# Kernel optimization log

Measured on AMD Instinct MI355X. Metric: run time of the kernel, lower is better.

## Reference

```python
import jax, jax.numpy as jnp
import numpy as np

NUM_HEADS = 8
DIM_HEAD = 48
SCALE = DIM_HEAD ** -0.5


def setup_inputs() -> dict:
    key = jax.random.key(0)
    k1, k2, k3 = jax.random.split(key, 3)
    B, N, D = 4, 2048, 384
    inner = NUM_HEADS * DIM_HEAD  # 384
    x = jax.random.normal(k1, (B, N, D), dtype=jnp.float32)
    # store weights in [in, out] layout (equivalent to torch Linear W.T)
    Wqkv = jax.random.normal(k2, (D, 3 * inner), dtype=jnp.float32) * (D ** -0.5)
    Wproj = jax.random.normal(k3, (inner, D), dtype=jnp.float32) * (inner ** -0.5)
    bproj = jnp.zeros((D,), dtype=jnp.float32)
    return {"x": x, "Wqkv": Wqkv, "Wproj": Wproj, "bproj": bproj}


def reference(x, Wqkv, Wproj, bproj):
    B, N, D = x.shape
    h, dh = NUM_HEADS, DIM_HEAD
    C = h * dh
    # fused QKV projection (qkv_bias=False)
    qkv = (x @ Wqkv).reshape(B, N, 3, h, dh)
    q = qkv[:, :, 0].transpose(0, 2, 1, 3)  # [B, h, N, dh]
    k = qkv[:, :, 1].transpose(0, 2, 1, 3)
    v = qkv[:, :, 2].transpose(0, 2, 1, 3)
    # naive attention: materialize [B, h, N, N] scores
    sim = jnp.einsum("bhqd,bhkd->bhqk", q, k) * SCALE
    attn = jax.nn.softmax(sim, axis=-1)
    out = jnp.einsum("bhqk,bhkd->bhqd", attn, v)  # [B, h, N, dh]
    out = out.transpose(0, 2, 1, 3).reshape(B, N, C)
    return out @ Wproj + bproj
```

## Files before the change

### kernel.cpp

```cpp
#include <hip/hip_runtime.h>
#include <hip/hip_bf16.h>


typedef _Float16 f16x8 __attribute__((ext_vector_type(8)));
typedef _Float16 f16x4 __attribute__((ext_vector_type(4)));
typedef _Float16 f16x2 __attribute__((ext_vector_type(2)));
typedef float    f32x4 __attribute__((ext_vector_type(4)));
typedef float    f32x16 __attribute__((ext_vector_type(16)));

#define QSCL 0.20822035963448658f

static __device__ __forceinline__ f16x2 cvt_pk_f16(float a, float b) {
    return __builtin_bit_cast(f16x2, __builtin_amdgcn_cvt_pkrtz(a, b));
}

__global__ __launch_bounds__(256) void prep(const float4* __restrict__ x,
                                            const float* __restrict__ wq,
                                            const float* __restrict__ wp,
                                            f16x4* __restrict__ xh4,
                                            _Float16* __restrict__ wqt,
                                            _Float16* __restrict__ wpt)
{
    __shared__ _Float16 t[64][65];
    const int blk = blockIdx.x, tid = threadIdx.x;
    if (blk < 144) {
        const float* src; _Float16* dst; int Nn, k0, n0;
        if (blk < 108) {
            src = wq; dst = wqt; Nn = 1152;
            k0 = (blk % 6) * 64; n0 = (blk / 6) * 64;
        } else {
            const int b2 = blk - 108;
            src = wp; dst = wpt; Nn = 384;
            k0 = (b2 % 6) * 64; n0 = (b2 / 6) * 64;
        }
        #pragma unroll
        for (int i = 0; i < 16; i++) {
            const int id = tid + i * 256;
            const int k = id >> 6, n = id & 63;
            t[k][n] = (_Float16)src[(size_t)(k0 + k) * Nn + n0 + n];
        }
        __syncthreads();
        #pragma unroll
        for (int i = 0; i < 16; i++) {
            const int id = tid + i * 256;
            const int n = id >> 6, k = id & 63;
            dst[(size_t)(n0 + n) * 384 + k0 + k] = t[k][n];
        }
    } else {
        const int base = (blk - 144) * 3072;
        #pragma unroll
        for (int r = 0; r < 12; r++) {
            const int j = base + r * 256 + tid;
            const float4 tt = x[j];
            f16x4 hh;
            hh[0] = (_Float16)tt.x; hh[1] = (_Float16)tt.y;
            hh[2] = (_Float16)tt.z; hh[3] = (_Float16)tt.w;
            xh4[j] = hh;
        }
    }
}

union QkvSmem {
    struct { _Float16 As[128][40]; _Float16 Bs[128][40]; } g;
    _Float16 Ts[128][136];
    _Float16 Ts2[128][136];
};

__global__ __launch_bounds__(256) void qkv_f16(const _Float16* __restrict__ A,
                                               const _Float16* __restrict__ Bt,
                                               _Float16* __restrict__ qh,
                                               _Float16* __restrict__ kh,
                                               _Float16* __restrict__ vt)
{
    __shared__ QkvSmem sm;
    const int tid = threadIdx.x;
    const int w = tid >> 6, lane = tid & 63, cl = lane & 15, quad = lane >> 4;
    const int bm = blockIdx.x, bn = blockIdx.y;

    f32x4 acc[2][8];
    const f32x4 z4 = {0.f, 0.f, 0.f, 0.f};
    #pragma unroll
    for (int mi = 0; mi < 2; mi++)
        #pragma unroll
        for (int t = 0; t < 8; t++) acc[mi][t] = z4;

    const int ar = tid >> 2, ac = (tid & 3) * 8;
    const _Float16* Ag = A  + (size_t)(bm * 128 + ar) * 384 + ac;
    const _Float16* Bg = Bt + (size_t)(bn * 128 + ar) * 384 + ac;

    f16x8 pa[2], pb[2];
    #pragma unroll
    for (int j = 0; j < 2; j++) {
        pa[j] = *(const f16x8*)(Ag + (size_t)(64 * j) * 384);
        pb[j] = *(const f16x8*)(Bg + (size_t)(64 * j) * 384);
    }

    for (int k0 = 0; k0 < 384; k0 += 32) {
        __syncthreads();
        #pragma unroll
        for (int j = 0; j < 2; j++) {
            *(f16x8*)&sm.g.As[ar + 64 * j][ac] = pa[j];
            *(f16x8*)&sm.g.Bs[ar + 64 * j][ac] = pb[j];
        }
        __syncthreads();
        if (k0 + 32 < 384) {
            #pragma unroll
            for (int j = 0; j < 2; j++) {
                pa[j] = *(const f16x8*)(Ag + (size_t)(64 * j) * 384 + k0 + 32);
                pb[j] = *(const f16x8*)(Bg + (size_t)(64 * j) * 384 + k0 + 32);
            }
        }
        f16x8 bf[8];
        #pragma unroll
        for (int t = 0; t < 8; t++)
            bf[t] = *(const f16x8*)&sm.g.Bs[t * 16 + cl][quad * 8];
        #pragma unroll
        for (int mi = 0; mi < 2; mi++) {
            const f16x8 af = *(const f16x8*)&sm.g.As[w * 32 + mi * 16 + cl][quad * 8];
            #pragma unroll
            for (int t = 0; t < 8; t++)
                acc[mi][t] = __builtin_amdgcn_mfma_f32_16x16x32_f16(af, bf[t], acc[mi][t], 0, 0, 0);
        }
    }

    const int s = (bn * 128) / 384;
    const int b  = (bm * 128) >> 11;
    const int n0 = (bm * 128) & 2047;
    if (s == 2) {
        __syncthreads();
        const int qp = ((quad & 1) << 1) | (quad >> 1);
        #pragma unroll
        for (int t = 0; t < 8; t++)
            #pragma unroll
            for (int mi = 0; mi < 2; mi++)
                #pragma unroll
                for (int r = 0; r < 4; r++)
                    sm.Ts[t * 16 + cl][w * 32 + mi * 16 + qp * 4 + r] =
                        (_Float16)acc[mi][t][r];
        __syncthreads();
        const int colbase = bn * 128 - 768;
        #pragma unroll
        for (int i = 0; i < 8; i++) {
            const int c = i * 256 + tid;
            const int col = c >> 4, nc = c & 15;
            const int gcol = colbase + col;
            const int head = gcol / 48, d = gcol - head * 48;
            const int bh = b * 8 + head;
            *(f16x8*)&vt[(size_t)(bh * 48 + d) * 2048 + n0 + nc * 8] =
                *(const f16x8*)&sm.Ts[col][nc * 8];
        }
    } else {
        __syncthreads();
        const float scl = (s == 0) ? QSCL : 1.0f;
        #pragma unroll
        for (int t = 0; t < 8; t++)
            #pragma unroll
            for (int mi = 0; mi < 2; mi++)
                #pragma unroll
                for (int r = 0; r < 4; r++)
                    sm.Ts2[w * 32 + mi * 16 + quad * 4 + r][t * 16 + cl] =
                        (_Float16)(acc[mi][t][r] * scl);
        __syncthreads();
        _Float16* dst = (s == 0) ? qh : kh;
        const int colbase = bn * 128 - s * 384;
        #pragma unroll
        for (int i = 0; i < 8; i++) {
            const int c = i * 256 + tid;
            const int row = c >> 4, ch = c & 15;
            const int gcol = colbase + ch * 8;
            const int head = gcol / 48, d = gcol - head * 48;
            const int bh = b * 8 + head;
            *(f16x8*)&dst[(size_t)(bh * 2048 + n0 + row) * 48 + d] =
                *(const f16x8*)&sm.Ts2[row][ch * 8];
        }
    }
}

#define KS_S 56
#define VS_S 72

union AttnSmem {
    struct {
        _Float16 Ks[2][2][64][KS_S];
        _Float16 Vts[2][2][64][VS_S];
    } a;
    struct {
        float    Of[128][52];
        float    lv[128];
        _Float16 Ot[128][58];
    } e;
};

__global__ __launch_bounds__(512) void attn_f16(const _Float16* __restrict__ qh,
                                                const _Float16* __restrict__ kh,
                                                const _Float16* __restrict__ vt,
                                                _Float16* __restrict__ ab)
{
    __shared__ AttnSmem sm;
    const int tid = threadIdx.x;
    const int w = tid >> 6, lane = tid & 63, ln = lane & 31, h = lane >> 5;
    const int g = w >> 2, wg = w & 3;
    const int tid2 = tid & 255;
    const int bh = blockIdx.x, qt = blockIdx.y;

    for (int i = tid; i < 2 * 2 * 16 * VS_S; i += 512) {
        const int gi = i / (2 * 16 * VS_S);
        const int j  = i - gi * (2 * 16 * VS_S);
        const int bi = j / (16 * VS_S);
        const int j2 = j - bi * (16 * VS_S);
        const int r = 48 + j2 / VS_S, c = j2 % VS_S;
        sm.a.Vts[gi][bi][r][c] = (r == 48) ? (_Float16)1.0f : (_Float16)0.0f;
    }

    f16x8 qf[3];
    {
        const _Float16* qp = qh + (size_t)(bh * 2048 + qt * 128 + wg * 32 + ln) * 48 + 8 * h;
        qf[0] = *(const f16x8*)qp;
        qf[1] = *(const f16x8*)(qp + 16);
        qf[2] = *(const f16x8*)(qp + 32);
    }

    f32x16 o0, o1;
    #pragma unroll
    for (int r = 0; r < 16; r++) { o0[r] = 0.f; o1[r] = 0.f; }

    const _Float16* kbase = kh + (size_t)bh * 2048 * 48 + (size_t)g * 1024 * 48;
    const _Float16* vbase = vt + (size_t)bh * 48 * 2048 + g * 1024;

    const int kr0 = tid2 / 6,        kc0 = (tid2 % 6) * 8;
    const int kid1 = tid2 + 256;
    const int kr1 = kid1 / 6,        kc1 = (kid1 % 6) * 8;
    const int vr0 = tid2 >> 3,       vc0 = (tid2 & 7) * 8;
    const int vr1 = vr0 + 32;
    const _Float16* ks0 = kbase + (size_t)kr0 * 48 + kc0;
    const _Float16* ks1 = kbase + (size_t)kr1 * 48 + kc1;
    const _Float16* vs0 = vbase + (size_t)vr0 * 2048 + vc0;
    const _Float16* vs1 = vbase + (size_t)vr1 * 2048 + vc0;

    f16x8 rk0 = *(const f16x8*)ks0;
    f16x8 rv0 = *(const f16x8*)vs0;
    f16x8 rk1, rv1;
    if (tid2 < 128) { rk1 = *(const f16x8*)ks1; rv1 = *(const f16x8*)vs1; }

    for (int t = 0; t < 16; ++t) {
        _Float16 (*Ksb)[KS_S] = sm.a.Ks[g][t & 1];
        _Float16 (*Vtb)[VS_S] = sm.a.Vts[g][t & 1];

        *(f16x8*)&Ksb[kr0][kc0] = rk0;
        *(f16x8*)&Vtb[vr0][vc0] = rv0;
        if (tid2 < 128) {
            *(f16x8*)&Ksb[kr1][kc1] = rk1;
            *(f16x8*)&Vtb[vr1][vc0] = rv1;
        }
        __syncthreads();

        if (t < 15) {
            const int off = (t + 1) * 64;
            rk0 = *(const f16x8*)(ks0 + (size_t)off * 48);
            rv0 = *(const f16x8*)(vs0 + off);
            if (tid2 < 128) {
                rk1 = *(const f16x8*)(ks1 + (size_t)off * 48);
                rv1 = *(const f16x8*)(vs1 + off);
            }
        }

        f32x16 s0, s1;
        #pragma unroll
        for (int r = 0; r < 16; r++) { s0[r] = 0.f; s1[r] = 0.f; }
        __builtin_amdgcn_s_setprio(1);
        #pragma unroll
        for (int i = 0; i < 3; i++) {
            const f16x8 ka0 = *(const f16x8*)&Ksb[ln][16 * i + 8 * h];
            s0 = __builtin_amdgcn_mfma_f32_32x32x16_f16(ka0, qf[i], s0, 0, 0, 0);
            const f16x8 ka1 = *(const f16x8*)&Ksb[32 + ln][16 * i + 8 * h];
            s1 = __builtin_amdgcn_mfma_f32_32x32x16_f16(ka1, qf[i], s1, 0, 0, 0);
        }
        __builtin_amdgcn_s_setprio(0);

        f16x8 pbf[4];
        f16x2* pp = (f16x2*)pbf;
        #pragma unroll
        for (int m = 0; m < 4; m++) {
            pp[m]      = cvt_pk_f16(
                __builtin_amdgcn_exp2f(s0[2 * m]),     __builtin_amdgcn_exp2f(s0[2 * m + 1]));
            pp[4 + m]  = cvt_pk_f16(
                __builtin_amdgcn_exp2f(s0[8 + 2 * m]), __builtin_amdgcn_exp2f(s0[9 + 2 * m]));
            pp[8 + m]  = cvt_pk_f16(
                __builtin_amdgcn_exp2f(s1[2 * m]),     __builtin_amdgcn_exp2f(s1[2 * m + 1]));
            pp[12 + m] = cvt_pk_f16(
                __builtin_amdgcn_exp2f(s1[8 + 2 * m]), __builtin_amdgcn_exp2f(s1[9 + 2 * m]));
        }

        __builtin_amdgcn_s_setprio(1);
        #pragma unroll
        for (int c = 0; c < 4; c++) {
            const f16x8 av0 = *(const f16x8*)&Vtb[ln][16 * c + 8 * h];
            o0 = __builtin_amdgcn_mfma_f32_32x32x16_f16(av0, pbf[c], o0, 0, 0, 0);
            const f16x8 av1 = *(const f16x8*)&Vtb[32 + ln][16 * c + 8 * h];
            o1 = __builtin_amdgcn_mfma_f32_32x32x16_f16(av1, pbf[c], o1, 0, 0, 0);
        }
        __builtin_amdgcn_s_setprio(0);
    }

    const float lown = __shfl(o1[8], ln);

    __syncthreads();

    const int row = wg * 32 + ln;
    if (g == 1) {
        #pragma unroll
        for (int q4 = 0; q4 < 4; q4++) {
            f32x4 tq = { o0[4 * q4], o0[4 * q4 + 1], o0[4 * q4 + 2], o0[4 * q4 + 3] };
            *(f32x4*)&sm.e.Of[row][8 * q4 + 4 * h] = tq;
        }
        #pragma unroll
        for (int q4 = 0; q4 < 2; q4++) {
            f32x4 tq = { o1[4 * q4], o1[4 * q4 + 1], o1[4 * q4 + 2], o1[4 * q4 + 3] };
            *(f32x4*)&sm.e.Of[row][32 + 8 * q4 + 4 * h] = tq;
        }
        if (h == 0) sm.e.lv[row] = o1[8];
    }
    __syncthreads();
    if (g == 0) {
        #pragma unroll
        for (int q4 = 0; q4 < 4; q4++) {
            const f32x4 tq = *(const f32x4*)&sm.e.Of[row][8 * q4 + 4 * h];
            o0[4 * q4] += tq[0]; o0[4 * q4 + 1] += tq[1];
            o0[4 * q4 + 2] += tq[2]; o0[4 * q4 + 3] += tq[3];
        }
        #pragma unroll
        for (int q4 = 0; q4 < 2; q4++) {
            const f32x4 tq = *(const f32x4*)&sm.e.Of[row][32 + 8 * q4 + 4 * h];
            o1[4 * q4] += tq[0]; o1[4 * q4 + 1] += tq[1];
            o1[4 * q4 + 2] += tq[2]; o1[4 * q4 + 3] += tq[3];
        }
        const float inv = 1.f / (lown + sm.e.lv[row]);
        #pragma unroll
        for (int r = 0; r < 16; r++)
            sm.e.Ot[row][(r & 3) + 8 * (r >> 2) + 4 * h] = (_Float16)(o0[r] * inv);
        #pragma unroll
        for (int r = 0; r < 8; r++)
            sm.e.Ot[row][32 + (r & 3) + 8 * (r >> 2) + 4 * h] = (_Float16)(o1[r] * inv);
    }
    __syncthreads();
    if (g == 0) {
        const int b = bh >> 3, hd = bh & 7;
        #pragma unroll
        for (int i = 0; i < 3; i++) {
            const int c2 = i * 256 + tid;
            const int rw = c2 / 6, ch = c2 % 6;
            const int q = qt * 128 + rw;
            *(f16x8*)&ab[(size_t)(b * 2048 + q) * 384 + hd * 48 + ch * 8] =
                *(const f16x8*)&sm.e.Ot[rw][ch * 8];
        }
    }
}

__global__ __launch_bounds__(256) void proj_f16(const _Float16* __restrict__ A,
                                                const _Float16* __restrict__ Bt,
                                                const float* __restrict__ bias,
                                                float* __restrict__ out)
{
    __shared__ _Float16 As[64][72];
    __shared__ _Float16 Bs[64][72];
    const int tid = threadIdx.x;
    const int w = tid >> 6, lane = tid & 63, cl = lane & 15, quad = lane >> 4;
    const int bm = blockIdx.x, bn = blockIdx.y;

    f32x4 acc[4];
    const f32x4 z4 = {0.f, 0.f, 0.f, 0.f};
    #pragma unroll
    for (int t = 0; t < 4; t++) acc[t] = z4;

    const int ar = tid >> 3, ac = (tid & 7) * 8;
    const _Float16* Ag = A  + (size_t)(bm * 64 + ar) * 384 + ac;
    const _Float16* Bg = Bt + (size_t)(bn * 64 + ar) * 384 + ac;

    f16x8 pa[2], pb[2];
    #pragma unroll
    for (int j = 0; j < 2; j++) {
        pa[j] = *(const f16x8*)(Ag + (size_t)(32 * j) * 384);
        pb[j] = *(const f16x8*)(Bg + (size_t)(32 * j) * 384);
    }

    for (int k0 = 0; k0 < 384; k0 += 64) {
        __syncthreads();
        #pragma unroll
        for (int j = 0; j < 2; j++) {
            *(f16x8*)&As[ar + 32 * j][ac] = pa[j];
            *(f16x8*)&Bs[ar + 32 * j][ac] = pb[j];
        }
        __syncthreads();
        if (k0 + 64 < 384) {
            #pragma unroll
            for (int j = 0; j < 2; j++) {
                pa[j] = *(const f16x8*)(Ag + (size_t)(32 * j) * 384 + k0 + 64);
                pb[j] = *(const f16x8*)(Bg + (size_t)(32 * j) * 384 + k0 + 64);
            }
        }
        #pragma unroll
        for (int kh2 = 0; kh2 < 2; kh2++) {
            const f16x8 af = *(const f16x8*)&As[w * 16 + cl][kh2 * 32 + quad * 8];
            #pragma unroll
            for (int t = 0; t < 4; t++) {
                const f16x8 bf = *(const f16x8*)&Bs[t * 16 + cl][kh2 * 32 + quad * 8];
                acc[t] = __builtin_amdgcn_mfma_f32_16x16x32_f16(af, bf, acc[t], 0, 0, 0);
            }
        }
    }

    #pragma unroll
    for (int t = 0; t < 4; t++) {
        const int col = bn * 64 + t * 16 + cl;
        const float bv = bias[col];
        #pragma unroll
        for (int r = 0; r < 4; r++) {
            const int row = bm * 64 + w * 16 + quad * 4 + r;
            out[(size_t)row * 384 + col] = acc[t][r] + bv;
        }
    }
}

extern "C" void kernel_launch(void* const* d_in, const int* in_sizes, int n_in,
                              void* d_out, int out_size, void* d_ws, size_t ws_size,
                              hipStream_t stream) {
    const float* x     = (const float*)d_in[0];
    const float* Wqkv  = (const float*)d_in[1];
    const float* Wproj = (const float*)d_in[2];
    const float* bproj = (const float*)d_in[3];
    float* out = (float*)d_out;

    char* ws = (char*)d_ws;
    _Float16* xh     = (_Float16*)(ws + 0);
    _Float16* wqkvt  = (_Float16*)(ws + 6291456);
    _Float16* wprojt = (_Float16*)(ws + 7176192);
    _Float16* qh     = (_Float16*)(ws + 7471104);
    _Float16* kh     = (_Float16*)(ws + 13762560);
    _Float16* vt     = (_Float16*)(ws + 20054016);
    _Float16* ab     = (_Float16*)(ws + 26345472);

    prep<<<400, 256, 0, stream>>>((const float4*)x, Wqkv, Wproj,
                                  (f16x4*)xh, wqkvt, wprojt);
    qkv_f16<<<dim3(64, 9), 256, 0, stream>>>(xh, wqkvt, qh, kh, vt);
    attn_f16<<<dim3(32, 16), 512, 0, stream>>>(qh, kh, vt, ab);
    proj_f16<<<dim3(128, 6), 256, 0, stream>>>(ab, wprojt, bproj, out);
}
```

Baseline: 130.2 us.

## Double-buffer LDS tiles to halve barriers in QKV, attention and projection

The QKV GEMM and projection GEMM now use two LDS buffers for their tiles, as the attention kernel already did for K/V. Each iteration writes the next tile into the other buffer before computing on the current one, so only one __syncthreads per iteration is needed instead of two. The global prefetch distance is pushed one more tile ahead. The projection kernel's K-step drops from 64 to 32 to fit the new layout, which raises the iteration count and the number of barriers it executes, and the doubled LDS footprint may affect occupancy.

New measurement: 128.7 us (median of 3 runs). About the same (-1.1%).

```diff
diff --git a/kernel.cpp b/kernel.cpp
--- a/kernel.cpp
+++ b/kernel.cpp
@@ -61,7 +61,7 @@
 }
 
 union QkvSmem {
-    struct { _Float16 As[128][40]; _Float16 Bs[128][40]; } g;
+    struct { _Float16 As[2][128][40]; _Float16 Bs[2][128][40]; } g;
     _Float16 Ts[128][136];
     _Float16 Ts2[128][136];
 };
@@ -94,40 +94,52 @@
         pa[j] = *(const f16x8*)(Ag + (size_t)(64 * j) * 384);
         pb[j] = *(const f16x8*)(Bg + (size_t)(64 * j) * 384);
     }
-
-    for (int k0 = 0; k0 < 384; k0 += 32) {
-        __syncthreads();
-        #pragma unroll
-        for (int j = 0; j < 2; j++) {
-            *(f16x8*)&sm.g.As[ar + 64 * j][ac] = pa[j];
-            *(f16x8*)&sm.g.Bs[ar + 64 * j][ac] = pb[j];
-        }
-        __syncthreads();
-        if (k0 + 32 < 384) {
+    #pragma unroll
+    for (int j = 0; j < 2; j++) {
+        *(f16x8*)&sm.g.As[0][ar + 64 * j][ac] = pa[j];
+        *(f16x8*)&sm.g.Bs[0][ar + 64 * j][ac] = pb[j];
+    }
+    #pragma unroll
+    for (int j = 0; j < 2; j++) {
+        pa[j] = *(const f16x8*)(Ag + (size_t)(64 * j) * 384 + 32);
+        pb[j] = *(const f16x8*)(Bg + (size_t)(64 * j) * 384 + 32);
+    }
+    __syncthreads();
+
+    for (int it = 0; it < 12; ++it) {
+        if (it < 11) {
             #pragma unroll
             for (int j = 0; j < 2; j++) {
-                pa[j] = *(const f16x8*)(Ag + (size_t)(64 * j) * 384 + k0 + 32);
-                pb[j] = *(const f16x8*)(Bg + (size_t)(64 * j) * 384 + k0 + 32);
+                *(f16x8*)&sm.g.As[(it + 1) & 1][ar + 64 * j][ac] = pa[j];
+                *(f16x8*)&sm.g.Bs[(it + 1) & 1][ar + 64 * j][ac] = pb[j];
             }
+            if (it < 10) {
+                const int off = (it + 2) * 32;
+                #pragma unroll
+                for (int j = 0; j < 2; j++) {
+                    pa[j] = *(const f16x8*)(Ag + (size_t)(64 * j) * 384 + off);
+                    pb[j] = *(const f16x8*)(Bg + (size_t)(64 * j) * 384 + off);
+                }
+            }
         }
         f16x8 bf[8];
         #pragma unroll
         for (int t = 0; t < 8; t++)
-            bf[t] = *(const f16x8*)&sm.g.Bs[t * 16 + cl][quad * 8];
+            bf[t] = *(const f16x8*)&sm.g.Bs[it & 1][t * 16 + cl][quad * 8];
         #pragma unroll
         for (int mi = 0; mi < 2; mi++) {
-            const f16x8 af = *(const f16x8*)&sm.g.As[w * 32 + mi * 16 + cl][quad * 8];
+            const f16x8 af = *(const f16x8*)&sm.g.As[it & 1][w * 32 + mi * 16 + cl][quad * 8];
             #pragma unroll
             for (int t = 0; t < 8; t++)
                 acc[mi][t] = __builtin_amdgcn_mfma_f32_16x16x32_f16(af, bf[t], acc[mi][t], 0, 0, 0);
         }
+        __syncthreads();
     }
 
     const int s = (bn * 128) / 384;
     const int b  = (bm * 128) >> 11;
     const int n0 = (bm * 128) & 2047;
     if (s == 2) {
-        __syncthreads();
         const int qp = ((quad & 1) << 1) | (quad >> 1);
         #pragma unroll
         for (int t = 0; t < 8; t++)
@@ -150,7 +162,6 @@
                 *(const f16x8*)&sm.Ts[col][nc * 8];
         }
     } else {
-        __syncthreads();
         const float scl = (s == 0) ? QSCL : 1.0f;
         #pragma unroll
         for (int t = 0; t < 8; t++)
@@ -242,27 +253,47 @@
     f16x8 rk1, rv1;
     if (tid2 < 128) { rk1 = *(const f16x8*)ks1; rv1 = *(const f16x8*)vs1; }
 
-    for (int t = 0; t < 16; ++t) {
-        _Float16 (*Ksb)[KS_S] = sm.a.Ks[g][t & 1];
-        _Float16 (*Vtb)[VS_S] = sm.a.Vts[g][t & 1];
-
+    {
+        _Float16 (*Ksb)[KS_S] = sm.a.Ks[g][0];
+        _Float16 (*Vtb)[VS_S] = sm.a.Vts[g][0];
         *(f16x8*)&Ksb[kr0][kc0] = rk0;
         *(f16x8*)&Vtb[vr0][vc0] = rv0;
         if (tid2 < 128) {
             *(f16x8*)&Ksb[kr1][kc1] = rk1;
             *(f16x8*)&Vtb[vr1][vc0] = rv1;
         }
-        __syncthreads();
-
+        rk0 = *(const f16x8*)(ks0 + (size_t)64 * 48);
+        rv0 = *(const f16x8*)(vs0 + 64);
+        if (tid2 < 128) {
+            rk1 = *(const f16x8*)(ks1 + (size_t)64 * 48);
+            rv1 = *(const f16x8*)(vs1 + 64);
+        }
+        __syncthreads();
+    }
+
+    for (int t = 0; t < 16; ++t) {
         if (t < 15) {
-            const int off = (t + 1) * 64;
-            rk0 = *(const f16x8*)(ks0 + (size_t)off * 48);
-            rv0 = *(const f16x8*)(vs0 + off);
+            _Float16 (*Ksn)[KS_S] = sm.a.Ks[g][(t + 1) & 1];
+            _Float16 (*Vtn)[VS_S] = sm.a.Vts[g][(t + 1) & 1];
+            *(f16x8*)&Ksn[kr0][kc0] = rk0;
+            *(f16x8*)&Vtn[vr0][vc0] = rv0;
             if (tid2 < 128) {
-                rk1 = *(const f16x8*)(ks1 + (size_t)off * 48);
-                rv1 = *(const f16x8*)(vs1 + off);
+                *(f16x8*)&Ksn[kr1][kc1] = rk1;
+                *(f16x8*)&Vtn[vr1][vc0] = rv1;
             }
-        }
+            if (t < 14) {
+                const int off = (t + 2) * 64;
+                rk0 = *(const f16x8*)(ks0 + (size_t)off * 48);
+                rv0 = *(const f16x8*)(vs0 + off);
+                if (tid2 < 128) {
+                    rk1 = *(const f16x8*)(ks1 + (size_t)off * 48);
+                    rv1 = *(const f16x8*)(vs1 + off);
+                }
+            }
+        }
+
+        _Float16 (*Ksb)[KS_S] = sm.a.Ks[g][t & 1];
+        _Float16 (*Vtb)[VS_S] = sm.a.Vts[g][t & 1];
 
         f32x16 s0, s1;
         #pragma unroll
@@ -300,11 +331,11 @@
             o1 = __builtin_amdgcn_mfma_f32_32x32x16_f16(av1, pbf[c], o1, 0, 0, 0);
         }
         __builtin_amdgcn_s_setprio(0);
+
+        __syncthreads();
     }
 
     const float lown = __shfl(o1[8], ln);
-
-    __syncthreads();
 
     const int row = wg * 32 + ln;
     if (g == 1) {
@@ -361,8 +392,8 @@
                                                 const float* __restrict__ bias,
                                                 float* __restrict__ out)
 {
-    __shared__ _Float16 As[64][72];
-    __shared__ _Float16 Bs[64][72];
+    __shared__ _Float16 As[2][64][40];
+    __shared__ _Float16 Bs[2][64][40];
     const int tid = threadIdx.x;
     const int w = tid >> 6, lane = tid & 63, cl = lane & 15, quad = lane >> 4;
     const int bm = blockIdx.x, bn = blockIdx.y;
@@ -372,41 +403,35 @@
     #pragma unroll
     for (int t = 0; t < 4; t++) acc[t] = z4;
 
-    const int ar = tid >> 3, ac = (tid & 7) * 8;
+    const int ar = tid >> 2, ac = (tid & 3) * 8;
     const _Float16* Ag = A  + (size_t)(bm * 64 + ar) * 384 + ac;
     const _Float16* Bg = Bt + (size_t)(bn * 64 + ar) * 384 + ac;
 
-    f16x8 pa[2], pb[2];
-    #pragma unroll
-    for (int j = 0; j < 2; j++) {
-        pa[j] = *(const f16x8*)(Ag + (size_t)(32 * j) * 384);
-        pb[j] = *(const f16x8*)(Bg + (size_t)(32 * j) * 384);
-    }
-
-    for (int k0 = 0; k0 < 384; k0 += 64) {
-        __syncthreads();
-        #pragma unroll
-        for (int j = 0; j < 2; j++) {
-            *(f16x8*)&As[ar + 32 * j][ac] = pa[j];
-            *(f16x8*)&Bs[ar + 32 * j][ac] = pb[j];
-        }
-        __syncthreads();
-        if (k0 + 64 < 384) {
-            #pragma unroll
-            for (int j = 0; j < 2; j++) {
-                pa[j] = *(const f16x8*)(Ag + (size_t)(32 * j) * 384 + k0 + 64);
-                pb[j] = *(const f16x8*)(Bg + (size_t)(32 * j) * 384 + k0 + 64);
+    f16x8 pa = *(const f16x8*)Ag;
+    f16x8 pb = *(const f16x8*)Bg;
+    *(f16x8*)&As[0][ar][ac] = pa;
+    *(f16x8*)&Bs[0][ar][ac] = pb;
+    pa = *(const f16x8*)(Ag + 32);
+    pb = *(const f16x8*)(Bg + 32);
+    __syncthreads();
+
+    for (int it = 0; it < 12; ++it) {
+        if (it < 11) {
+            *(f16x8*)&As[(it + 1) & 1][ar][ac] = pa;
+            *(f16x8*)&Bs[(it + 1) & 1][ar][ac] = pb;
+            if (it < 10) {
+                const int off = (it + 2) * 32;
+                pa = *(const f16x8*)(Ag + off);
+                pb = *(const f16x8*)(Bg + off);
             }
         }
-        #pragma unroll
-        for (int kh2 = 0; kh2 < 2; kh2++) {
-            const f16x8 af = *(const f16x8*)&As[w * 16 + cl][kh2 * 32 + quad * 8];
-            #pragma unroll
-            for (int t = 0; t < 4; t++) {
-                const f16x8 bf = *(const f16x8*)&Bs[t * 16 + cl][kh2 * 32 + quad * 8];
-                acc[t] = __builtin_amdgcn_mfma_f32_16x16x32_f16(af, bf, acc[t], 0, 0, 0);
-            }
-        }
+        const f16x8 af = *(const f16x8*)&As[it & 1][w * 16 + cl][quad * 8];
+        #pragma unroll
+        for (int t = 0; t < 4; t++) {
+            const f16x8 bf = *(const f16x8*)&Bs[it & 1][t * 16 + cl][quad * 8];
+            acc[t] = __builtin_amdgcn_mfma_f32_16x16x32_f16(af, bf, acc[t], 0, 0, 0);
+        }
+        __syncthreads();
     }
 
     #pragma unroll
```
